# Optimization experiments

Hardware: AMD Instinct MI355X
Metric: run time of the kernel (lower is better)

## Reference

```python
import jax, jax.numpy as jnp
import numpy as np

SEQ_LEN = 1024
D_MODEL = 512
K_FILT = 24
HEADS = 8
R = 512  # must equal d_model for the module's forward to type-check
NFFT = 2048  # nearest power of two >= 2*SEQ_LEN-1
LN_EPS = 1e-5


def _spectral_filters():
    # Hankel matrix Z[i,j] = 2 / ((i+j)^3 - (i+j)), i,j in 1..T
    e = np.arange(1, SEQ_LEN + 1, dtype=np.float64)
    ipj = e[:, None] + e[None, :]
    Z = 2.0 / (ipj ** 3 - ipj)
    sigma, phi = np.linalg.eigh(Z)
    sigma_k = np.clip(sigma[-K_FILT:], 1e-9, None)
    phi_k = phi[:, -K_FILT:] * sigma_k ** 0.25
    return phi_k.astype(np.float32)  # (T, K)


def setup_inputs() -> dict:
    key = jax.random.key(0)
    ks = jax.random.split(key, 12)
    s = 0.02
    B = 2

    def lin(k):
        kw, kb = jax.random.split(k)
        return (jax.random.normal(kw, (D_MODEL, D_MODEL), jnp.float32) * s,
                jax.random.normal(kb, (D_MODEL,), jnp.float32) * s)

    Wq, bq = lin(ks[0]); Wk, bk = lin(ks[1]); Wv, bv = lin(ks[2])
    Wg, bg = lin(ks[3]); Wo, bo = lin(ks[4])
    return {
        'x': jax.random.normal(ks[5], (B, SEQ_LEN, D_MODEL), jnp.float32),
        'stu_filters': jnp.asarray(_spectral_filters()),
        'M_inputs': jax.random.normal(ks[6], (D_MODEL, R), jnp.float32) * s,
        'M_filters': jax.random.normal(ks[7], (K_FILT, R), jnp.float32) * s,
        'Wq': Wq, 'bq': bq, 'Wk': Wk, 'bk': bk, 'Wv': Wv, 'bv': bv,
        'Wg': Wg, 'bg': bg, 'Wo': Wo, 'bo': bo,
        'ln_w': jnp.ones((R,), jnp.float32),
        'ln_b': jnp.zeros((R,), jnp.float32),
    }


def _stu_conv(u, v):
    # u: (B, T, r), v: (T, r). FFT-based causal conv with sign featurization.
    T = u.shape[1]
    sgn = jnp.where(jnp.arange(T) % 2 == 1, -1.0, 1.0)[None, :, None]  # (1,T,1)
    Vf = jnp.fft.rfft(v[None, :, :, None], n=NFFT, axis=1)  # (1,F,r,1)
    U = jnp.stack([u, u * sgn], axis=-1)  # (B,T,r,2)
    Uf = jnp.fft.rfft(U, n=NFFT, axis=1)  # (B,F,r,2)
    conv = jnp.fft.irfft(Vf * Uf, n=NFFT, axis=1)[:, :T]  # (B,T,r,2)
    return conv[..., 0], conv[..., 1] * sgn


def _layernorm(x, w, b):
    mu = jnp.mean(x, axis=-1, keepdims=True)
    var = jnp.mean((x - mu) ** 2, axis=-1, keepdims=True)
    return (x - mu) * jax.lax.rsqrt(var + LN_EPS) * w + b


def reference(x, stu_filters, M_inputs, M_filters, Wq, bq, Wk, bk, Wv, bv,
              Wg, bg, Wo, bo, ln_w, ln_b):
    B, T, d = x.shape
    hd = d // HEADS
    # STU features
    u_proj = x @ M_inputs                    # (B,T,r)
    phi_proj = stu_filters @ M_filters       # (T,r)
    sp, sm = _stu_conv(u_proj, phi_proj)
    x_tilde = _layernorm(sp + sm, ln_w, ln_b)  # (B,T,r==d)
    # gated linear attention with gelu features and causal cumsum state
    def proj(W, b):
        y = (x @ W.T + b).reshape(B, T, HEADS, hd).transpose(0, 2, 1, 3)
        return jax.nn.gelu(y, approximate=True)
    Q = proj(Wq, bq); K = proj(Wk, bk); V = proj(Wv, bv)
    Zt = jnp.einsum('bhtp,bhtn->bhtpn', V, K)   # (B,H,T,hd,hd)
    Hc = jnp.cumsum(Zt, axis=2)
    Y = jnp.einsum('bhtp,bhtpn->bhtn', Q, Hc)   # (B,H,T,hd)
    Y_attn = Y.transpose(0, 2, 1, 3).reshape(B, T, d)
    gate = jax.nn.sigmoid(x @ Wg.T + bg)
    comb = gate * Y_attn + (1.0 - gate) * x_tilde
    return comb @ Wo.T + bo
```

## Files before the change

kernel.cpp:

```cpp
#include <hip/hip_runtime.h>
#include <hip/hip_bf16.h>

#define T_SEQ 1024
#define D_MOD 512
#define NHEAD 8
#define HDIM  64
#define R_DIM 512
#define BATCH 2

typedef __attribute__((ext_vector_type(8))) __bf16 bf16x8;
typedef __attribute__((ext_vector_type(4))) __bf16 bf16x4;
typedef __attribute__((ext_vector_type(4))) float f32x4;

__device__ __forceinline__ float ldin(const void* p, size_t i, int bf) {
    if (bf) return __bfloat162float(((const __hip_bfloat16*)p)[i]);
    return ((const float*)p)[i];
}
__device__ __forceinline__ void stout(void* p, size_t i, int bf, float v) {
    if (bf) ((__hip_bfloat16*)p)[i] = __float2bfloat16(v);
    else    ((float*)p)[i] = v;
}

__device__ __forceinline__ float gelu_f(float x) {
    return 0.5f * x * (1.f + tanhf(0.7978845608028654f * (x + 0.044715f * x * x * x)));
}

__device__ __forceinline__ bf16x8 cvt8(float4 a, float4 b) {
    bf16x8 t;
    t[0]=(__bf16)a.x; t[1]=(__bf16)a.y; t[2]=(__bf16)a.z; t[3]=(__bf16)a.w;
    t[4]=(__bf16)b.x; t[5]=(__bf16)b.y; t[6]=(__bf16)b.z; t[7]=(__bf16)b.w;
    return t;
}

template<int BF>
__global__ __launch_bounds__(256) void mega_gemm(
    const void* __restrict__ x, const void* __restrict__ Mi,
    const void* __restrict__ stf, const void* __restrict__ Mf,
    const void* __restrict__ Wq, const void* __restrict__ bq,
    const void* __restrict__ Wk, const void* __restrict__ bk,
    const void* __restrict__ Wv, const void* __restrict__ bv,
    const void* __restrict__ Wg, const void* __restrict__ bg,
    __bf16* __restrict__ fu, __bf16* __restrict__ fphi,
    __bf16* __restrict__ fQ, __bf16* __restrict__ fKT,
    __bf16* __restrict__ fV, __bf16* __restrict__ fG)
{
    constexpr int bf = BF;
    const int tid = threadIdx.x;
    const int z = blockIdx.z;
    const int m0 = blockIdx.y * 64;
    const int n0 = blockIdx.x * 64;

    __shared__ __align__(16) __bf16 As[64][40];
    __shared__ __align__(16) __bf16 Bs[2][64][40];
    const int wave = tid >> 6, lane = tid & 63;
    const int lm = lane & 15, kq = lane >> 4;
    const int mo = tid >> 2, ko = (tid & 3) * 8;

    if (z <= 1) {
        const void* Wp0 = (z == 0) ? Wq : Wv;
        const void* Wp1 = (z == 0) ? Wk : Wg;
        const void* bp0 = (z == 0) ? bq : bv;
        const void* bp1 = (z == 0) ? bk : bg;
        f32x4 acc[2][4] = {};
        const int cs = ((((ko >> 3) ^ (mo >> 3)) & 3) << 3);

        for (int k0 = 0; k0 < 512; k0 += 32) {
            if (k0) __syncthreads();
            if (bf) {
                *(bf16x8*)&As[mo][ko] =
                    *(const bf16x8*)((const __bf16*)x + (size_t)(m0 + mo) * 512 + k0 + ko);
            } else {
                const float* Af = (const float*)x + (size_t)(m0 + mo) * 512 + k0 + ko;
                *(bf16x8*)&As[mo][ko] = cvt8(*(const float4*)Af, *(const float4*)(Af + 4));
            }
            const size_t go = (size_t)(n0 + mo) * 512 + k0 + ko;
            if (bf) {
                *(bf16x8*)&Bs[0][mo][cs] = *(const bf16x8*)((const __bf16*)Wp0 + go);
                *(bf16x8*)&Bs[1][mo][cs] = *(const bf16x8*)((const __bf16*)Wp1 + go);
            } else {
                const float* B0 = (const float*)Wp0 + go;
                const float* B1 = (const float*)Wp1 + go;
                *(bf16x8*)&Bs[0][mo][cs] = cvt8(*(const float4*)B0, *(const float4*)(B0 + 4));
                *(bf16x8*)&Bs[1][mo][cs] = cvt8(*(const float4*)B1, *(const float4*)(B1 + 4));
            }
            __syncthreads();
            const bf16x8 a = *(const bf16x8*)&As[wave * 16 + lm][kq * 8];
            #pragma unroll
            for (int p = 0; p < 2; ++p) {
                #pragma unroll
                for (int nt = 0; nt < 4; ++nt) {
                    const int row = nt * 16 + lm;
                    const bf16x8 b = *(const bf16x8*)&Bs[p][row][(((kq ^ (row >> 3)) & 3) << 3)];
                    acc[p][nt] = __builtin_amdgcn_mfma_f32_16x16x32_bf16(a, b, acc[p][nt], 0, 0, 0);
                }
            }
        }
        #pragma unroll
        for (int p = 0; p < 2; ++p) {
            const void* bias = p ? bp1 : bp0;
            #pragma unroll
            for (int nt = 0; nt < 4; ++nt) {
                const int n = n0 + nt * 16 + lm;
                #pragma unroll
                for (int r2 = 0; r2 < 4; ++r2) {
                    const int m = m0 + wave * 16 + kq * 4 + r2;
                    float v = acc[p][nt][r2] + ldin(bias, (size_t)n, bf);
                    v = (z == 1 && p == 1) ? 1.f / (1.f + expf(-v)) : gelu_f(v);
                    if (z == 0) {
                        if (p == 0) fQ[(size_t)m * 512 + n] = (__bf16)v;
                        else {
                            const int b = m >> 10, t = m & 1023;
                            const int h = n >> 6,  pp = n & 63;
                            fKT[(((size_t)b * NHEAD + h) * 64 + pp) * T_SEQ + t] = (__bf16)v;
                        }
                    } else {
                        if (p == 0) fV[(size_t)m * 512 + n] = (__bf16)v;
                        else        fG[(size_t)m * 512 + n] = (__bf16)v;
                    }
                }
            }
        }
    } else if (z == 2) {
        f32x4 acc[4] = {};
        const int kk = tid >> 3, nn = (tid & 7) * 8;
        for (int k0 = 0; k0 < 512; k0 += 32) {
            if (k0) __syncthreads();
            if (bf) {
                *(bf16x8*)&As[mo][ko] =
                    *(const bf16x8*)((const __bf16*)x + (size_t)(m0 + mo) * 512 + k0 + ko);
            } else {
                const float* Af = (const float*)x + (size_t)(m0 + mo) * 512 + k0 + ko;
                *(bf16x8*)&As[mo][ko] = cvt8(*(const float4*)Af, *(const float4*)(Af + 4));
            }
            {
                const size_t off = (size_t)(k0 + kk) * 512 + n0 + nn;
                bf16x8 t;
                if (bf) {
                    t = *(const bf16x8*)((const __bf16*)Mi + off);
                } else {
                    const float* Bf = (const float*)Mi + off;
                    t = cvt8(*(const float4*)Bf, *(const float4*)(Bf + 4));
                }
                #pragma unroll
                for (int q = 0; q < 8; ++q) {
                    const int row = nn + q;
                    const int c = ((((kk >> 3) ^ (row >> 3)) & 3) << 3) | (kk & 7);
                    Bs[0][row][c] = t[q];
                }
            }
            __syncthreads();
            const bf16x8 a = *(const bf16x8*)&As[wave * 16 + lm][kq * 8];
            #pragma unroll
            for (int nt = 0; nt < 4; ++nt) {
                const int row = nt * 16 + lm;
                const bf16x8 b = *(const bf16x8*)&Bs[0][row][(((kq ^ (row >> 3)) & 3) << 3)];
                acc[nt] = __builtin_amdgcn_mfma_f32_16x16x32_bf16(a, b, acc[nt], 0, 0, 0);
            }
        }
        #pragma unroll
        for (int nt = 0; nt < 4; ++nt) {
            const int n = n0 + nt * 16 + lm;
            #pragma unroll
            for (int r2 = 0; r2 < 4; ++r2) {
                const int m = m0 + wave * 16 + kq * 4 + r2;
                fu[(size_t)m * 512 + n] = (__bf16)acc[nt][r2];
            }
        }
    } else {
        if (blockIdx.y >= 16) {
            float4* zp = (float4*)(fphi + 524288);
            const int bid = (blockIdx.y - 16) * 8 + blockIdx.x;
            const float4 z4 = make_float4(0.f, 0.f, 0.f, 0.f);
            #pragma unroll
            for (int q = 0; q < 16; ++q)
                zp[(size_t)bid * 4096 + q * 256 + tid] = z4;
            return;
        }
        f32x4 acc[4] = {};
        const int kk = tid >> 3, nn = (tid & 7) * 8;
        {
            bf16x8 t;
            #pragma unroll
            for (int q = 0; q < 8; ++q) {
                const int k = ko + q;
                t[q] = (k < 24) ? (__bf16)ldin(stf, (size_t)(m0 + mo) * 24 + k, bf)
                                : (__bf16)0.f;
            }
            *(bf16x8*)&As[mo][ko] = t;
        }
        #pragma unroll
        for (int q = 0; q < 8; ++q) {
            const int row = nn + q;
            const int c = ((((kk >> 3) ^ (row >> 3)) & 3) << 3) | (kk & 7);
            Bs[0][row][c] = (kk < 24) ? (__bf16)ldin(Mf, (size_t)kk * 512 + n0 + row, bf)
                                      : (__bf16)0.f;
        }
        __syncthreads();
        const bf16x8 a = *(const bf16x8*)&As[wave * 16 + lm][kq * 8];
        #pragma unroll
        for (int nt = 0; nt < 4; ++nt) {
            const int row = nt * 16 + lm;
            const bf16x8 b = *(const bf16x8*)&Bs[0][row][(((kq ^ (row >> 3)) & 3) << 3)];
            acc[nt] = __builtin_amdgcn_mfma_f32_16x16x32_bf16(a, b, acc[nt], 0, 0, 0);
        }
        #pragma unroll
        for (int nt = 0; nt < 4; ++nt) {
            const int n = n0 + nt * 16 + lm;
            #pragma unroll
            for (int r2 = 0; r2 < 4; ++r2) {
                const int m = m0 + wave * 16 + kq * 4 + r2;
                fphi[(size_t)m * 512 + n] = (__bf16)acc[nt][r2];
            }
        }
    }
}

__global__ __launch_bounds__(256) void conv_attn_k(
    const __bf16* __restrict__ u, const __bf16* __restrict__ vphi,
    float* __restrict__ w,
    const __bf16* __restrict__ Q, const __bf16* __restrict__ KT,
    const __bf16* __restrict__ V, float* __restrict__ Y)
{
    __shared__ __align__(16) unsigned char smem[49152];
    const int tid = threadIdx.x;
    const int z = blockIdx.z;
    int rem = blockIdx.x, ti = 0;
    while (rem >= ((ti + 4) >> 2)) { rem -= (ti + 4) >> 2; ++ti; }
    const int jlo = rem * 4;
    const int jhi = (jlo + 3 < ti) ? jlo + 3 : ti;
    const int t0 = ti * 64;

    if (z < 2) {
        float (*vs)[64] = (float (*)[64])smem;
        float (*us)[64] = (float (*)[64])(smem + 16384);
        const int rl = tid & 63, tg = tid >> 6;
        const int b = z;
        const int r0 = blockIdx.y * 64;
        const __bf16* ub = u + (size_t)b * T_SEQ * R_DIM;
        float acc[16] = {};
        for (int j = jlo; j <= jhi; ++j) {
            if (j != jlo) __syncthreads();
            const int L0 = j * 64;
            const int W0 = t0 - L0 - 63;
            #pragma unroll
            for (int jj = 0; jj < 8; ++jj) {
                const int n = jj * 256 + tid;
                const int row = n >> 4, c4 = (n & 15) * 4;
                int s = W0 + row;
                s = s < 0 ? 0 : (s > T_SEQ - 1 ? T_SEQ - 1 : s);
                const bf16x4 t = *(const bf16x4*)&ub[(size_t)s * R_DIM + r0 + c4];
                *(float4*)&us[row][c4] =
                    make_float4((float)t[0], (float)t[1], (float)t[2], (float)t[3]);
            }
            #pragma unroll
            for (int jj = 0; jj < 4; ++jj) {
                const int n = jj * 256 + tid;
                const int row = n >> 4, c4 = (n & 15) * 4;
                const bf16x4 t = *(const bf16x4*)&vphi[(size_t)(L0 + row) * R_DIM + r0 + c4];
                *(float4*)&vs[row][c4] =
                    make_float4((float)t[0], (float)t[1], (float)t[2], (float)t[3]);
            }
            __syncthreads();
            if (j < ti) {
                #pragma unroll
                for (int g = 0; g < 4; ++g) {
                    const int wsmin = tg * 16 + 49 - 16 * g;
                    float ur[30];
                    #pragma unroll
                    for (int q = 0; q < 30; ++q) ur[q] = us[wsmin + q][rl];
                    float vr[8];
                    #pragma unroll
                    for (int e = 0; e < 8; ++e) vr[e] = vs[16 * g + 2 * e][rl];
                    #pragma unroll
                    for (int e = 0; e < 8; ++e)
                        #pragma unroll
                        for (int i = 0; i < 16; ++i)
                            acc[i] += vr[e] * ur[i - 2 * e + 14];
                }
            } else {
                for (int l = 0; l < 64; l += 2) {
                    const float vv = vs[l][rl];
                    #pragma unroll
                    for (int i = 0; i < 16; ++i) {
                        const int srel = tg * 16 + i - l;
                        if (srel >= 0) acc[i] += vv * us[srel + 63][rl];
                    }
                }
            }
        }
        #pragma unroll
        for (int i = 0; i < 16; ++i)
            atomicAdd(&w[((size_t)b * T_SEQ + t0 + tg * 16 + i) * R_DIM + r0 + rl],
                      2.f * acc[i]);
    } else {
        __bf16 (*Qs)[72] = (__bf16 (*)[72])smem;
        __bf16 (*Vs)[72] = (__bf16 (*)[72])(smem + 9216);
        __bf16 (*Kt)[72] = (__bf16 (*)[72])(smem + 18432);
        __bf16 (*Sa)[72] = (__bf16 (*)[72])(smem + 27648);
        const int wave = tid >> 6, lane = tid & 63;
        const int lm = lane & 15, kq = lane >> 4;
        const int b = z - 2;
        const int h = blockIdx.y;
        const size_t cbase = ((size_t)b * T_SEQ) * D_MOD + h * HDIM;
        const __bf16* KTh = KT + (((size_t)b * NHEAD + h) * 64) * T_SEQ;
        #pragma unroll
        for (int it = 0; it < 2; ++it) {
            const int n = it * 256 + tid;
            const int row = n >> 3, p0 = (n & 7) * 8;
            *(bf16x8*)&Qs[row][p0] = *(const bf16x8*)&Q[cbase + (size_t)(t0 + row) * D_MOD + p0];
        }
        f32x4 accY[4] = {};
        for (int j = jlo; j <= jhi; ++j) {
            const int s0 = j * 64;
            __syncthreads();
            #pragma unroll
            for (int it = 0; it < 2; ++it) {
                const int n = it * 256 + tid;
                const int row = n >> 3, c0 = (n & 7) * 8;
                *(bf16x8*)&Vs[row][c0] = *(const bf16x8*)&V[cbase + (size_t)(s0 + row) * D_MOD + c0];
                *(bf16x8*)&Kt[row][c0] = *(const bf16x8*)&KTh[(size_t)row * T_SEQ + s0 + c0];
            }
            __syncthreads();
            f32x4 sacc[4] = {};
            #pragma unroll
            for (int ks = 0; ks < 2; ++ks) {
                const bf16x8 a = *(const bf16x8*)&Qs[wave * 16 + lm][ks * 32 + kq * 8];
                #pragma unroll
                for (int nt = 0; nt < 4; ++nt) {
                    const bf16x8 bb = *(const bf16x8*)&Vs[nt * 16 + lm][ks * 32 + kq * 8];
                    sacc[nt] = __builtin_amdgcn_mfma_f32_16x16x32_bf16(a, bb, sacc[nt], 0, 0, 0);
                }
            }
            const bool diag = (j == ti);
            #pragma unroll
            for (int nt = 0; nt < 4; ++nt) {
                const int sl = nt * 16 + lm;
                #pragma unroll
                for (int r2 = 0; r2 < 4; ++r2) {
                    const int tl = wave * 16 + kq * 4 + r2;
                    float v = sacc[nt][r2];
                    if (diag && sl > tl) v = 0.f;
                    Sa[tl][sl] = (__bf16)v;
                }
            }
            #pragma unroll
            for (int ks = 0; ks < 2; ++ks) {
                const bf16x8 a = *(const bf16x8*)&Sa[wave * 16 + lm][ks * 32 + kq * 8];
                #pragma unroll
                for (int nt = 0; nt < 4; ++nt) {
                    const bf16x8 bb = *(const bf16x8*)&Kt[nt * 16 + lm][ks * 32 + kq * 8];
                    accY[nt] = __builtin_amdgcn_mfma_f32_16x16x32_bf16(a, bb, accY[nt], 0, 0, 0);
                }
            }
        }
        #pragma unroll
        for (int nt = 0; nt < 4; ++nt) {
            const int nh = nt * 16 + lm;
            #pragma unroll
            for (int r2 = 0; r2 < 4; ++r2) {
                const int tl = wave * 16 + kq * 4 + r2;
                atomicAdd(&Y[cbase + (size_t)(t0 + tl) * D_MOD + nh], accY[nt][r2]);
            }
        }
    }
}

__global__ __launch_bounds__(256) void stats_k(const float* __restrict__ w,
                                               float* __restrict__ stats)
{
    const int tid = threadIdx.x;
    const int r = tid >> 4, c = tid & 15;
    const int row = blockIdx.x * 16 + r;
    const float* p = w + (size_t)row * R_DIM;
    float s = 0.f, ss = 0.f;
    #pragma unroll
    for (int q = 0; q < 8; ++q) {
        const float4 v = *(const float4*)(p + c * 4 + q * 64);
        s  += v.x + v.y + v.z + v.w;
        ss += v.x * v.x + v.y * v.y + v.z * v.z + v.w * v.w;
    }
    s  += __shfl_xor(s, 1, 64);  s  += __shfl_xor(s, 2, 64);
    s  += __shfl_xor(s, 4, 64);  s  += __shfl_xor(s, 8, 64);
    ss += __shfl_xor(ss, 1, 64); ss += __shfl_xor(ss, 2, 64);
    ss += __shfl_xor(ss, 4, 64); ss += __shfl_xor(ss, 8, 64);
    if (c == 0) {
        const float mu = s * (1.f / 512.f);
        float var = ss * (1.f / 512.f) - mu * mu;
        var = var < 0.f ? 0.f : var;
        stats[row * 2]     = mu;
        stats[row * 2 + 1] = rsqrtf(var + 1e-5f);
    }
}

template<int BF>
__global__ __launch_bounds__(256) void final_gemm(const __bf16* __restrict__ G,
                                                  const float* __restrict__ Yf,
                                                  const float* __restrict__ Wf,
                                                  const float* __restrict__ stats,
                                                  const void* __restrict__ lnw,
                                                  const void* __restrict__ lnb,
                                                  const void* __restrict__ Wo,
                                                  const void* __restrict__ bo,
                                                  void* __restrict__ out)
{
    constexpr int bf = BF;
    __shared__ __align__(16) __bf16 sm[2][2 * 64 * 40];
    const int tid = threadIdx.x;
    const int wave = tid >> 6, lane = tid & 63;
    const int lm = lane & 15, kq = lane >> 4;
    const int mo = tid >> 2, ko = (tid & 3) * 8;
    const int m0 = blockIdx.y * 64, n0 = blockIdx.x * 64;

    const float2 st = *(const float2*)(stats + (size_t)(m0 + mo) * 2);
    const float mu = st.x, rs = st.y;

    bf16x8 pg, pw, pLg, pLb;
    float4 py0, py1, pv0, pv1, pw0, pw1, pLg0, pLg1, pLb0, pLb1;

    auto issue = [&](int k0) {
        const size_t off = (size_t)(m0 + mo) * 512 + k0 + ko;
        pg  = *(const bf16x8*)(G + off);
        py0 = *(const float4*)(Yf + off); py1 = *(const float4*)(Yf + off + 4);
        pv0 = *(const float4*)(Wf + off); pv1 = *(const float4*)(Wf + off + 4);
        const size_t ob = (size_t)(n0 + mo) * 512 + k0 + ko;
        if (bf) {
            pw  = *(const bf16x8*)((const __bf16*)Wo + ob);
            pLg = *(const bf16x8*)((const __bf16*)lnw + k0 + ko);
            pLb = *(const bf16x8*)((const __bf16*)lnb + k0 + ko);
        } else {
            const float* Bf = (const float*)Wo + ob;
            pw0 = *(const float4*)Bf; pw1 = *(const float4*)(Bf + 4);
            const float* Lg = (const float*)lnw + k0 + ko;
            pLg0 = *(const float4*)Lg; pLg1 = *(const float4*)(Lg + 4);
            const float* Lb = (const float*)lnb + k0 + ko;
            pLb0 = *(const float4*)Lb; pLb1 = *(const float4*)(Lb + 4);
        }
    };
    auto commit = [&](int bi) {
        __bf16 (*As)[40] = (__bf16 (*)[40])sm[bi];
        __bf16 (*Bs)[40] = (__bf16 (*)[40])(sm[bi] + 64 * 40);
        const float yv[8] = {py0.x,py0.y,py0.z,py0.w,py1.x,py1.y,py1.z,py1.w};
        const float wv[8] = {pv0.x,pv0.y,pv0.z,pv0.w,pv1.x,pv1.y,pv1.z,pv1.w};
        float gw[8], gb[8];
        if (bf) {
            #pragma unroll
            for (int q = 0; q < 8; ++q) { gw[q] = (float)pLg[q]; gb[q] = (float)pLb[q]; }
        } else {
            gw[0]=pLg0.x; gw[1]=pLg0.y; gw[2]=pLg0.z; gw[3]=pLg0.w;
            gw[4]=pLg1.x; gw[5]=pLg1.y; gw[6]=pLg1.z; gw[7]=pLg1.w;
            gb[0]=pLb0.x; gb[1]=pLb0.y; gb[2]=pLb0.z; gb[3]=pLb0.w;
            gb[4]=pLb1.x; gb[5]=pLb1.y; gb[6]=pLb1.z; gb[7]=pLb1.w;
        }
        bf16x8 t;
        #pragma unroll
        for (int q = 0; q < 8; ++q) {
            const float xt = (wv[q] - mu) * rs * gw[q] + gb[q];
            const float gg = (float)pg[q];
            t[q] = (__bf16)(gg * yv[q] + (1.f - gg) * xt);
        }
        *(bf16x8*)&As[mo][ko] = t;
        *(bf16x8*)&Bs[mo][ko] = bf ? pw : cvt8(pw0, pw1);
    };

    f32x4 acc[4] = {};
    issue(0);
    commit(0);
    __syncthreads();
    int cur = 0;
    for (int k0 = 0; k0 < 512; k0 += 32) {
        const bool haveNext = (k0 + 32 < 512);
        if (haveNext) issue(k0 + 32);
        __bf16 (*As)[40] = (__bf16 (*)[40])sm[cur];
        __bf16 (*Bs)[40] = (__bf16 (*)[40])(sm[cur] + 64 * 40);
        const bf16x8 a = *(const bf16x8*)&As[wave * 16 + lm][kq * 8];
        #pragma unroll
        for (int nt = 0; nt < 4; ++nt) {
            const bf16x8 b = *(const bf16x8*)&Bs[nt * 16 + lm][kq * 8];
            acc[nt] = __builtin_amdgcn_mfma_f32_16x16x32_bf16(a, b, acc[nt], 0, 0, 0);
        }
        if (haveNext) {
            commit(cur ^ 1);
            __syncthreads();
            cur ^= 1;
        }
    }
    #pragma unroll
    for (int nt = 0; nt < 4; ++nt) {
        const int n = n0 + nt * 16 + lm;
        #pragma unroll
        for (int r2 = 0; r2 < 4; ++r2) {
            const int m = m0 + wave * 16 + kq * 4 + r2;
            float v = acc[nt][r2] + ldin(bo, (size_t)n, bf);
            stout(out, (size_t)m * 512 + n, bf, v);
        }
    }
}

extern "C" void kernel_launch(void* const* d_in, const int* in_sizes, int n_in,
                              void* d_out, int out_size, void* d_ws, size_t ws_size,
                              hipStream_t stream)
{
    const void* x   = d_in[0];
    const void* stf = d_in[1];
    const void* Mi  = d_in[2];
    const void* Mf  = d_in[3];
    const void* Wq  = d_in[4];  const void* bq = d_in[5];
    const void* Wk  = d_in[6];  const void* bk = d_in[7];
    const void* Wv  = d_in[8];  const void* bv = d_in[9];
    const void* Wg  = d_in[10]; const void* bg = d_in[11];
    const void* Wo  = d_in[12]; const void* bo = d_in[13];
    const void* lnw = d_in[14]; const void* lnb = d_in[15];

    float* base = (float*)d_ws;
    __bf16* f_u   = (__bf16*)base;
    __bf16* f_phi = f_u + 1048576;
    float*  f_w   = base + 786432;
    float*  f_Y   = base + 1835008;
    __bf16* f_Q   = (__bf16*)(base + 3407872);
    __bf16* f_KT  = f_Q + 1048576;
    __bf16* f_V   = f_KT + 1048576;
    __bf16* f_G   = f_V + 1048576;
    float*  f_st  = (float*)(f_G + 1048576);

    const int bf = (in_sizes[0] == BATCH * T_SEQ * D_MOD * 2);

    dim3 blk(256);

    if (bf)
        mega_gemm<1><<<dim3(8, 32, 4), blk, 0, stream>>>(
            x, Mi, stf, Mf, Wq, bq, Wk, bk, Wv, bv, Wg, bg,
            f_u, f_phi, f_Q, f_KT, f_V, f_G);
    else
        mega_gemm<0><<<dim3(8, 32, 4), blk, 0, stream>>>(
            x, Mi, stf, Mf, Wq, bq, Wk, bk, Wv, bv, Wg, bg,
            f_u, f_phi, f_Q, f_KT, f_V, f_G);

    conv_attn_k<<<dim3(40, 8, 4), blk, 0, stream>>>(f_u, f_phi, f_w, f_Q, f_KT, f_V, f_Y);

    stats_k<<<dim3(128), blk, 0, stream>>>(f_w, f_st);

    if (bf) final_gemm<1><<<dim3(8, 32), blk, 0, stream>>>(f_G, f_Y, f_w, f_st, lnw, lnb, Wo, bo, d_out);
    else    final_gemm<0><<<dim3(8, 32), blk, 0, stream>>>(f_G, f_Y, f_w, f_st, lnw, lnb, Wo, bo, d_out);
}
```

Before: 165.5 us.

## Replace quadratic causal attention tiles with chunked state prefix sums

Linear attention is restructured into chunks. A new kernel computes a per-chunk K^T V state for each 64-step chunk. The attention part of conv_attn_k then handles only its diagonal chunk intra-chunk and adds Q times the prefix sum of the earlier chunk states. The old version looped over all earlier key chunks and accumulated Y with atomics. Y is now written directly as bf16, with no atomics or zero-init, and final_gemm reads the bf16 Y. The cost is an extra transposed V store, an extra kernel launch, serial fp32 prefix summation of up to 15 states per block, and lower precision in Y.

```diff
diff --git a/kernel.cpp b/kernel.cpp
--- a/kernel.cpp
+++ b/kernel.cpp
@@ -42,7 +42,8 @@
     const void* __restrict__ Wg, const void* __restrict__ bg,
     __bf16* __restrict__ fu, __bf16* __restrict__ fphi,
     __bf16* __restrict__ fQ, __bf16* __restrict__ fKT,
-    __bf16* __restrict__ fV, __bf16* __restrict__ fG)
+    __bf16* __restrict__ fV, __bf16* __restrict__ fVT,
+    __bf16* __restrict__ fG)
 {
     constexpr int bf = BF;
     const int tid = threadIdx.x;
@@ -106,16 +107,18 @@
                     const int m = m0 + wave * 16 + kq * 4 + r2;
                     float v = acc[p][nt][r2] + ldin(bias, (size_t)n, bf);
                     v = (z == 1 && p == 1) ? 1.f / (1.f + expf(-v)) : gelu_f(v);
+                    const int b = m >> 10, t = m & 1023;
+                    const int h = n >> 6,  pp = n & 63;
                     if (z == 0) {
                         if (p == 0) fQ[(size_t)m * 512 + n] = (__bf16)v;
-                        else {
-                            const int b = m >> 10, t = m & 1023;
-                            const int h = n >> 6,  pp = n & 63;
-                            fKT[(((size_t)b * NHEAD + h) * 64 + pp) * T_SEQ + t] = (__bf16)v;
+                        else fKT[(((size_t)b * NHEAD + h) * 64 + pp) * T_SEQ + t] = (__bf16)v;
+                    } else {
+                        if (p == 0) {
+                            fV[(size_t)m * 512 + n] = (__bf16)v;
+                            fVT[(((size_t)b * NHEAD + h) * 64 + pp) * T_SEQ + t] = (__bf16)v;
+                        } else {
+                            fG[(size_t)m * 512 + n] = (__bf16)v;
                         }
-                    } else {
-                        if (p == 0) fV[(size_t)m * 512 + n] = (__bf16)v;
-                        else        fG[(size_t)m * 512 + n] = (__bf16)v;
                     }
                 }
             }
@@ -172,8 +175,8 @@
             const int bid = (blockIdx.y - 16) * 8 + blockIdx.x;
             const float4 z4 = make_float4(0.f, 0.f, 0.f, 0.f);
             #pragma unroll
-            for (int q = 0; q < 16; ++q)
-                zp[(size_t)bid * 4096 + q * 256 + tid] = z4;
+            for (int q = 0; q < 8; ++q)
+                zp[(size_t)bid * 2048 + q * 256 + tid] = z4;
             return;
         }
         f32x4 acc[4] = {};
@@ -215,22 +218,67 @@
     }
 }
 
+__global__ __launch_bounds__(256) void state_k(const __bf16* __restrict__ KT,
+                                               const __bf16* __restrict__ VT,
+                                               float* __restrict__ T)
+{
+    __shared__ __align__(16) __bf16 Kt[64][72];
+    __shared__ __align__(16) __bf16 Vt[64][72];
+    const int tid = threadIdx.x;
+    const int ti = blockIdx.x, h = blockIdx.y, b = blockIdx.z;
+    const int s0 = ti * 64;
+    const int wave = tid >> 6, lane = tid & 63;
+    const int lm = lane & 15, kq = lane >> 4;
+    const size_t hb = (size_t)b * NHEAD + h;
+    const __bf16* KTh = KT + hb * 64 * T_SEQ;
+    const __bf16* VTh = VT + hb * 64 * T_SEQ;
+    #pragma unroll
+    for (int it = 0; it < 2; ++it) {
+        const int n = it * 256 + tid;
+        const int row = n >> 3, c0 = (n & 7) * 8;
+        *(bf16x8*)&Kt[row][c0] = *(const bf16x8*)&KTh[(size_t)row * T_SEQ + s0 + c0];
+        *(bf16x8*)&Vt[row][c0] = *(const bf16x8*)&VTh[(size_t)row * T_SEQ + s0 + c0];
+    }
+    __syncthreads();
+    f32x4 acc[4] = {};
+    #pragma unroll
+    for (int ks = 0; ks < 2; ++ks) {
+        const bf16x8 a = *(const bf16x8*)&Kt[wave * 16 + lm][ks * 32 + kq * 8];
+        #pragma unroll
+        for (int nt = 0; nt < 4; ++nt) {
+            const bf16x8 bb = *(const bf16x8*)&Vt[nt * 16 + lm][ks * 32 + kq * 8];
+            acc[nt] = __builtin_amdgcn_mfma_f32_16x16x32_bf16(a, bb, acc[nt], 0, 0, 0);
+        }
+    }
+    float* Tt = T + (hb * 16 + ti) * 4096;
+    #pragma unroll
+    for (int nt = 0; nt < 4; ++nt) {
+        const int p = nt * 16 + lm;
+        #pragma unroll
+        for (int r2 = 0; r2 < 4; ++r2) {
+            const int n = wave * 16 + kq * 4 + r2;
+            Tt[n * 64 + p] = acc[nt][r2];
+        }
+    }
+}
+
 __global__ __launch_bounds__(256) void conv_attn_k(
     const __bf16* __restrict__ u, const __bf16* __restrict__ vphi,
     float* __restrict__ w,
     const __bf16* __restrict__ Q, const __bf16* __restrict__ KT,
-    const __bf16* __restrict__ V, float* __restrict__ Y)
+    const __bf16* __restrict__ V, const float* __restrict__ T,
+    __bf16* __restrict__ Yb)
 {
     __shared__ __align__(16) unsigned char smem[49152];
     const int tid = threadIdx.x;
     const int z = blockIdx.z;
-    int rem = blockIdx.x, ti = 0;
-    while (rem >= ((ti + 4) >> 2)) { rem -= (ti + 4) >> 2; ++ti; }
-    const int jlo = rem * 4;
-    const int jhi = (jlo + 3 < ti) ? jlo + 3 : ti;
-    const int t0 = ti * 64;
 
     if (z < 2) {
+        int rem = blockIdx.x, ti = 0;
+        while (rem >= ((ti + 4) >> 2)) { rem -= (ti + 4) >> 2; ++ti; }
+        const int jlo = rem * 4;
+        const int jhi = (jlo + 3 < ti) ? jlo + 3 : ti;
+        const int t0 = ti * 64;
         float (*vs)[64] = (float (*)[64])smem;
         float (*us)[64] = (float (*)[64])(smem + 16384);
         const int rl = tid & 63, tg = tid >> 6;
@@ -293,62 +341,88 @@
             atomicAdd(&w[((size_t)b * T_SEQ + t0 + tg * 16 + i) * R_DIM + r0 + rl],
                       2.f * acc[i]);
     } else {
+        const int ti = blockIdx.x;
+        if (ti >= 16) return;
+        const int t0 = ti * 64;
         __bf16 (*Qs)[72] = (__bf16 (*)[72])smem;
         __bf16 (*Vs)[72] = (__bf16 (*)[72])(smem + 9216);
         __bf16 (*Kt)[72] = (__bf16 (*)[72])(smem + 18432);
         __bf16 (*Sa)[72] = (__bf16 (*)[72])(smem + 27648);
+        __bf16 (*PB)[72] = (__bf16 (*)[72])(smem + 36864);
         const int wave = tid >> 6, lane = tid & 63;
         const int lm = lane & 15, kq = lane >> 4;
         const int b = z - 2;
         const int h = blockIdx.y;
+        const size_t hb = (size_t)b * NHEAD + h;
         const size_t cbase = ((size_t)b * T_SEQ) * D_MOD + h * HDIM;
-        const __bf16* KTh = KT + (((size_t)b * NHEAD + h) * 64) * T_SEQ;
+        const __bf16* KTh = KT + hb * 64 * T_SEQ;
+
         #pragma unroll
         for (int it = 0; it < 2; ++it) {
             const int n = it * 256 + tid;
-            const int row = n >> 3, p0 = (n & 7) * 8;
-            *(bf16x8*)&Qs[row][p0] = *(const bf16x8*)&Q[cbase + (size_t)(t0 + row) * D_MOD + p0];
+            const int row = n >> 3, c0 = (n & 7) * 8;
+            *(bf16x8*)&Qs[row][c0] = *(const bf16x8*)&Q[cbase + (size_t)(t0 + row) * D_MOD + c0];
+            *(bf16x8*)&Vs[row][c0] = *(const bf16x8*)&V[cbase + (size_t)(t0 + row) * D_MOD + c0];
+            *(bf16x8*)&Kt[row][c0] = *(const bf16x8*)&KTh[(size_t)row * T_SEQ + t0 + c0];
+        }
+        {
+            const int mo = tid >> 2, ko2 = (tid & 3) * 16;
+            float ps[16] = {};
+            const float* Tb = T + hb * 16 * 4096 + mo * 64 + ko2;
+            for (int j = 0; j < ti; ++j) {
+                const float* tj = Tb + (size_t)j * 4096;
+                #pragma unroll
+                for (int q = 0; q < 4; ++q) {
+                    const float4 v = *(const float4*)(tj + q * 4);
+                    ps[q*4+0] += v.x; ps[q*4+1] += v.y; ps[q*4+2] += v.z; ps[q*4+3] += v.w;
+                }
+            }
+            bf16x8 t0v, t1v;
+            #pragma unroll
+            for (int q = 0; q < 8; ++q) { t0v[q] = (__bf16)ps[q]; t1v[q] = (__bf16)ps[8+q]; }
+            *(bf16x8*)&PB[mo][ko2]     = t0v;
+            *(bf16x8*)&PB[mo][ko2 + 8] = t1v;
+        }
+        __syncthreads();
+
+        f32x4 sacc[4] = {};
+        #pragma unroll
+        for (int ks = 0; ks < 2; ++ks) {
+            const bf16x8 a = *(const bf16x8*)&Qs[wave * 16 + lm][ks * 32 + kq * 8];
+            #pragma unroll
+            for (int nt = 0; nt < 4; ++nt) {
+                const bf16x8 bb = *(const bf16x8*)&Vs[nt * 16 + lm][ks * 32 + kq * 8];
+                sacc[nt] = __builtin_amdgcn_mfma_f32_16x16x32_bf16(a, bb, sacc[nt], 0, 0, 0);
+            }
+        }
+        #pragma unroll
+        for (int nt = 0; nt < 4; ++nt) {
+            const int sl = nt * 16 + lm;
+            #pragma unroll
+            for (int r2 = 0; r2 < 4; ++r2) {
+                const int tl = wave * 16 + kq * 4 + r2;
+                float v = sacc[nt][r2];
+                if (sl > tl) v = 0.f;
+                Sa[tl][sl] = (__bf16)v;
+            }
         }
         f32x4 accY[4] = {};
-        for (int j = jlo; j <= jhi; ++j) {
-            const int s0 = j * 64;
-            __syncthreads();
-            #pragma unroll
-            for (int it = 0; it < 2; ++it) {
-                const int n = it * 256 + tid;
-                const int row = n >> 3, c0 = (n & 7) * 8;
-                *(bf16x8*)&Vs[row][c0] = *(const bf16x8*)&V[cbase + (size_t)(s0 + row) * D_MOD + c0];
-                *(bf16x8*)&Kt[row][c0] = *(const bf16x8*)&KTh[(size_t)row * T_SEQ + s0 + c0];
-            }
-            __syncthreads();
-            f32x4 sacc[4] = {};
+        #pragma unroll
+        for (int ks = 0; ks < 2; ++ks) {
+            const bf16x8 a = *(const bf16x8*)&Sa[wave * 16 + lm][ks * 32 + kq * 8];
+            #pragma unroll
+            for (int nt = 0; nt < 4; ++nt) {
+                const bf16x8 bb = *(const bf16x8*)&Kt[nt * 16 + lm][ks * 32 + kq * 8];
+                accY[nt] = __builtin_amdgcn_mfma_f32_16x16x32_bf16(a, bb, accY[nt], 0, 0, 0);
+            }
+        }
+        if (ti) {
             #pragma unroll
             for (int ks = 0; ks < 2; ++ks) {
                 const bf16x8 a = *(const bf16x8*)&Qs[wave * 16 + lm][ks * 32 + kq * 8];
                 #pragma unroll
                 for (int nt = 0; nt < 4; ++nt) {
-                    const bf16x8 bb = *(const bf16x8*)&Vs[nt * 16 + lm][ks * 32 + kq * 8];
-                    sacc[nt] = __builtin_amdgcn_mfma_f32_16x16x32_bf16(a, bb, sacc[nt], 0, 0, 0);
-                }
-            }
-            const bool diag = (j == ti);
-            #pragma unroll
-            for (int nt = 0; nt < 4; ++nt) {
-                const int sl = nt * 16 + lm;
-                #pragma unroll
-                for (int r2 = 0; r2 < 4; ++r2) {
-                    const int tl = wave * 16 + kq * 4 + r2;
-                    float v = sacc[nt][r2];
-                    if (diag && sl > tl) v = 0.f;
-                    Sa[tl][sl] = (__bf16)v;
-                }
-            }
-            #pragma unroll
-            for (int ks = 0; ks < 2; ++ks) {
-                const bf16x8 a = *(const bf16x8*)&Sa[wave * 16 + lm][ks * 32 + kq * 8];
-                #pragma unroll
-                for (int nt = 0; nt < 4; ++nt) {
-                    const bf16x8 bb = *(const bf16x8*)&Kt[nt * 16 + lm][ks * 32 + kq * 8];
+                    const bf16x8 bb = *(const bf16x8*)&PB[nt * 16 + lm][ks * 32 + kq * 8];
                     accY[nt] = __builtin_amdgcn_mfma_f32_16x16x32_bf16(a, bb, accY[nt], 0, 0, 0);
                 }
             }
@@ -359,7 +433,7 @@
             #pragma unroll
             for (int r2 = 0; r2 < 4; ++r2) {
                 const int tl = wave * 16 + kq * 4 + r2;
-                atomicAdd(&Y[cbase + (size_t)(t0 + tl) * D_MOD + nh], accY[nt][r2]);
+                Yb[cbase + (size_t)(t0 + tl) * D_MOD + nh] = (__bf16)accY[nt][r2];
             }
         }
     }
@@ -394,7 +468,7 @@
 
 template<int BF>
 __global__ __launch_bounds__(256) void final_gemm(const __bf16* __restrict__ G,
-                                                  const float* __restrict__ Yf,
+                                                  const __bf16* __restrict__ Yf,
                                                   const float* __restrict__ Wf,
                                                   const float* __restrict__ stats,
                                                   const void* __restrict__ lnw,
@@ -414,13 +488,13 @@
     const float2 st = *(const float2*)(stats + (size_t)(m0 + mo) * 2);
     const float mu = st.x, rs = st.y;
 
-    bf16x8 pg, pw, pLg, pLb;
-    float4 py0, py1, pv0, pv1, pw0, pw1, pLg0, pLg1, pLb0, pLb1;
+    bf16x8 pg, py, pw, pLg, pLb;
+    float4 pv0, pv1, pw0, pw1, pLg0, pLg1, pLb0, pLb1;
 
     auto issue = [&](int k0) {
         const size_t off = (size_t)(m0 + mo) * 512 + k0 + ko;
         pg  = *(const bf16x8*)(G + off);
-        py0 = *(const float4*)(Yf + off); py1 = *(const float4*)(Yf + off + 4);
+        py  = *(const bf16x8*)(Yf + off);
         pv0 = *(const float4*)(Wf + off); pv1 = *(const float4*)(Wf + off + 4);
         const size_t ob = (size_t)(n0 + mo) * 512 + k0 + ko;
         if (bf) {
@@ -439,7 +513,6 @@
     auto commit = [&](int bi) {
         __bf16 (*As)[40] = (__bf16 (*)[40])sm[bi];
         __bf16 (*Bs)[40] = (__bf16 (*)[40])(sm[bi] + 64 * 40);
-        const float yv[8] = {py0.x,py0.y,py0.z,py0.w,py1.x,py1.y,py1.z,py1.w};
         const float wv[8] = {pv0.x,pv0.y,pv0.z,pv0.w,pv1.x,pv1.y,pv1.z,pv1.w};
         float gw[8], gb[8];
         if (bf) {
@@ -456,7 +529,7 @@
         for (int q = 0; q < 8; ++q) {
             const float xt = (wv[q] - mu) * rs * gw[q] + gb[q];
             const float gg = (float)pg[q];
-            t[q] = (__bf16)(gg * yv[q] + (1.f - gg) * xt);
+            t[q] = (__bf16)(gg * (float)py[q] + (1.f - gg) * xt);
         }
         *(bf16x8*)&As[mo][ko] = t;
         *(bf16x8*)&Bs[mo][ko] = bf ? pw : cvt8(pw0, pw1);
@@ -515,12 +588,14 @@
     __bf16* f_u   = (__bf16*)base;
     __bf16* f_phi = f_u + 1048576;
     float*  f_w   = base + 786432;
-    float*  f_Y   = base + 1835008;
+    float*  f_T   = base + 1835008;
+    __bf16* f_VT  = (__bf16*)(base + 2883584);
     __bf16* f_Q   = (__bf16*)(base + 3407872);
     __bf16* f_KT  = f_Q + 1048576;
     __bf16* f_V   = f_KT + 1048576;
     __bf16* f_G   = f_V + 1048576;
     float*  f_st  = (float*)(f_G + 1048576);
+    __bf16* f_Yb  = (__bf16*)(f_st + 4096);
 
     const int bf = (in_sizes[0] == BATCH * T_SEQ * D_MOD * 2);
 
@@ -529,16 +604,18 @@
     if (bf)
         mega_gemm<1><<<dim3(8, 32, 4), blk, 0, stream>>>(
             x, Mi, stf, Mf, Wq, bq, Wk, bk, Wv, bv, Wg, bg,
-            f_u, f_phi, f_Q, f_KT, f_V, f_G);
+            f_u, f_phi, f_Q, f_KT, f_V, f_VT, f_G);
     else
         mega_gemm<0><<<dim3(8, 32, 4), blk, 0, stream>>>(
             x, Mi, stf, Mf, Wq, bq, Wk, bk, Wv, bv, Wg, bg,
-            f_u, f_phi, f_Q, f_KT, f_V, f_G);
-
-    conv_attn_k<<<dim3(40, 8, 4), blk, 0, stream>>>(f_u, f_phi, f_w, f_Q, f_KT, f_V, f_Y);
+            f_u, f_phi, f_Q, f_KT, f_V, f_VT, f_G);
+
+    state_k<<<dim3(16, 8, 2), blk, 0, stream>>>(f_KT, f_VT, f_T);
+
+    conv_attn_k<<<dim3(40, 8, 4), blk, 0, stream>>>(f_u, f_phi, f_w, f_Q, f_KT, f_V, f_T, f_Yb);
 
     stats_k<<<dim3(128), blk, 0, stream>>>(f_w, f_st);
 
-    if (bf) final_gemm<1><<<dim3(8, 32), blk, 0, stream>>>(f_G, f_Y, f_w, f_st, lnw, lnb, Wo, bo, d_out);
-    else    final_gemm<0><<<dim3(8, 32), blk, 0, stream>>>(f_G, f_Y, f_w, f_st, lnw, lnb, Wo, bo, d_out);
-}
+    if (bf) final_gemm<1><<<dim3(8, 32), blk, 0, stream>>>(f_G, f_Yb, f_w, f_st, lnw, lnb, Wo, bo, d_out);
+    else    final_gemm<0><<<dim3(8, 32), blk, 0, stream>>>(f_G, f_Yb, f_w, f_st, lnw, lnb, Wo, bo, d_out);
+}
```

Result: no change. 167.4 us (+1.1%).
